# Kernel tuning notes

Hardware: AMD Instinct MI355X
Metric: run time of the kernel (lower is better)

Reference implementation:

```python
import jax, jax.numpy as jnp
import numpy as np

B, C, H, W = 8, 3, 1024, 1024
N, D, PS, NB, NH = 512, 256, 16, 8, 4


def _bin_matrix():
    # static radial-binning averaging matrix for a PS x (PS//2+1) rfft2 spectrum
    h, w = PS, PS // 2 + 1
    fy = np.fft.fftfreq(h)
    fx = np.linspace(0.0, 0.5, w)
    r = np.sqrt(fx[None, :] ** 2 + fy[:, None] ** 2)
    max_r = r.max() + 1e-6
    edges = np.linspace(0.0, max_r, NB + 1)
    idx = np.clip(np.searchsorted(edges, r.ravel(), side='right') - 1, 0, NB - 1)
    M = np.zeros((NB, h * w), np.float32)
    M[idx, np.arange(h * w)] = 1.0
    cnt = M.sum(1, keepdims=True)
    return M / np.maximum(cnt, 1.0)

_BIN_M = jnp.asarray(_bin_matrix())


def _ln(x, g, b, eps=1e-5):
    m = x.mean(-1, keepdims=True)
    v = x.var(-1, keepdims=True)
    return g * (x - m) / jnp.sqrt(v + eps) + b


def _gelu(x):
    return jax.nn.gelu(x, approximate=False)


def setup_inputs() -> dict:
    key = jax.random.key(0)
    ks = jax.random.split(key, 16)
    xav = lambda k, o, i: (jax.random.normal(k, (o, i)) / np.sqrt(i)).astype(jnp.float32)
    z = lambda n: jnp.zeros((n,), jnp.float32)
    o1 = lambda n: jnp.ones((n,), jnp.float32)
    FD = 2 * NB
    return {
        'image': jax.random.normal(ks[0], (B, C, H, W), jnp.float32),
        'point_coords': jax.random.uniform(ks[1], (B, N, 2), jnp.float32, 0.0, float(W)),
        'point_labels': jax.random.randint(ks[2], (B, N), 0, 2),
        'pe_w': xav(ks[3], D, D), 'pe_b': z(D),
        'type_emb': (0.02 * jax.random.normal(ks[4], (2, D))).astype(jnp.float32),
        'fbi': (1.0 + 0.1 * jax.random.normal(ks[5], (NB,))).astype(jnp.float32),
        'fe1_w': xav(ks[6], D // 2, FD), 'fe1_b': z(D // 2),
        'feln1_g': o1(D // 2), 'feln1_b': z(D // 2),
        'fe2_w': xav(ks[7], D, D // 2), 'fe2_b': z(D),
        'feln2_g': o1(D), 'feln2_b': z(D),
        'in_w': xav(ks[8], 3 * D, D), 'in_b': z(3 * D),
        'ao_w': xav(ks[9], D, D), 'ao_b': z(D),
        'n1_g': o1(D), 'n1_b': z(D),
        'f1_w': xav(ks[10], 2 * D, D), 'f1_b': z(2 * D),
        'f2_w': xav(ks[11], D, 2 * D), 'f2_b': z(D),
        'n2_g': o1(D), 'n2_b': z(D),
        'op_w': xav(ks[12], D, D), 'op_b': z(D),
    }


def reference(image, point_coords, point_labels, pe_w, pe_b, type_emb, fbi,
              fe1_w, fe1_b, feln1_g, feln1_b, fe2_w, fe2_b, feln2_g, feln2_b,
              in_w, in_b, ao_w, ao_b, n1_g, n1_b, f1_w, f1_b, f2_w, f2_b,
              n2_g, n2_b, op_w, op_b):
    Bv, Cv, Hv, Wv = image.shape
    Nv = point_coords.shape[1]
    # --- sinusoidal positional encoding (SAM style) + linear proj ---
    nc = point_coords / jnp.array([Wv, Hv], jnp.float32)
    dim_t = 10000.0 ** (2.0 * jnp.arange(D // 4, dtype=jnp.float32) / (D // 4))
    ax = (nc[..., 0:1] * (2.0 * np.pi)) / dim_t          # [B,N,D/4]
    ay = (nc[..., 1:2] * (2.0 * np.pi)) / dim_t
    pe = jnp.concatenate([jnp.sin(ax), jnp.cos(ax), jnp.sin(ay), jnp.cos(ay)], -1)
    spatial = pe @ pe_w.T + pe_b + type_emb[point_labels]  # [B,N,D]
    # --- batched per-point patch gather + rfft2 + radial binning ---
    gray = image.mean(1)                                   # [B,H,W]
    pc = jax.lax.stop_gradient(point_coords)               # .long() detaches in torch
    half = PS // 2
    px = jnp.clip(pc[..., 0].astype(jnp.int32), half, Wv - half - 1)
    py = jnp.clip(pc[..., 1].astype(jnp.int32), half, Hv - half - 1)
    off = jnp.arange(PS) - half
    rows = py[..., None] + off                             # [B,N,PS]
    cols = px[..., None] + off
    bidx = jnp.arange(Bv)[:, None, None, None]
    patches = gray[bidx, rows[..., :, None], cols[..., None, :]]  # [B,N,PS,PS]
    fft = jnp.fft.rfft2(patches, norm='ortho')             # [B,N,PS,PS//2+1]
    mag_bins = jnp.abs(fft).reshape(Bv, Nv, -1) @ _BIN_M.T    # [B,N,NB]
    ph_bins = jnp.angle(fft).reshape(Bv, Nv, -1) @ _BIN_M.T
    feat = jnp.concatenate([mag_bins * jax.nn.softmax(fbi), ph_bins], -1)  # [B,N,2*NB]
    # --- freq encoder MLP ---
    h1 = _gelu(_ln(feat @ fe1_w.T + fe1_b, feln1_g, feln1_b))
    freq = _ln(h1 @ fe2_w.T + fe2_b, feln2_g, feln2_b)     # [B,N,D]
    # --- cross-attention fusion (spatial = Q, freq = K/V) ---
    hd = D // NH
    q = (spatial @ in_w[:D].T + in_b[:D]).reshape(Bv, Nv, NH, hd)
    k = (freq @ in_w[D:2 * D].T + in_b[D:2 * D]).reshape(Bv, Nv, NH, hd)
    v = (freq @ in_w[2 * D:].T + in_b[2 * D:]).reshape(Bv, Nv, NH, hd)
    att = jax.nn.softmax(jnp.einsum('bqhd,bkhd->bhqk', q, k) / np.sqrt(hd), -1)
    o = jnp.einsum('bhqk,bkhd->bqhd', att, v).reshape(Bv, Nv, D)
    x = _ln(spatial + (o @ ao_w.T + ao_b), n1_g, n1_b)
    ffn = _gelu(x @ f1_w.T + f1_b) @ f2_w.T + f2_b
    x = _ln(x + ffn, n2_g, n2_b)
    return x @ op_w.T + op_b
```

## Files before the change

### kernel.cpp

```cpp
#include <hip/hip_runtime.h>
#include <math.h>


typedef __attribute__((ext_vector_type(8))) short short8;
typedef __attribute__((ext_vector_type(4))) float floatx4;
typedef unsigned short u16;
typedef unsigned long long u64;

__device__ __forceinline__ float gelu_f(float x) {
  return 0.5f * x * (1.0f + erff(x * 0.70710678118654752f));
}

__device__ __forceinline__ u16 bf16_rn(float x) {
  union { float f; unsigned u; } v; v.f = x;
  unsigned r = v.u + 0x7fffu + ((v.u >> 16) & 1u);
  return (u16)(r >> 16);
}

__device__ __forceinline__ void split_bf16(float x, u16& h, u16& l) {
  h = bf16_rn(x);
  union { unsigned u; float f; } hv; hv.u = ((unsigned)h) << 16;
  l = bf16_rn(x - hv.f);
}

#define W_PE   0
#define W_FE1  65536
#define W_FE2  67584
#define W_IN   100352
#define W_AO   296960
#define W_F1   362496
#define W_F2   493568
#define W_OP   624640


template <int NA, int K>
__device__ __forceinline__ void mm16_swz(
    const u16* Ah, const u16* Al, const int S,
    const u16* __restrict__ Bh, const u16* __restrict__ Bl,
    floatx4* acc)
{
  const int t = threadIdx.x;
  const int w = t >> 6, lane = t & 63;
  const int lm = lane & 15, kg = lane >> 4;
  #pragma unroll
  for (int it = 0; it < K / 32; ++it) {
    const short8 a_h = *(const short8*)&Ah[lm * S + it * 32 + kg * 8];
    const short8 a_l = *(const short8*)&Al[lm * S + it * 32 + kg * 8];
    #pragma unroll
    for (int nj = 0; nj < NA; nj++) {
      const size_t wo = (size_t)(((w * NA + nj) * (K / 32) + it) * 512 + lane * 8);
      const short8 b_h = *(const short8*)&Bh[wo];
      const short8 b_l = *(const short8*)&Bl[wo];
      acc[nj] = __builtin_amdgcn_mfma_f32_16x16x32_bf16(a_h, b_h, acc[nj], 0, 0, 0);
      acc[nj] = __builtin_amdgcn_mfma_f32_16x16x32_bf16(a_h, b_l, acc[nj], 0, 0, 0);
      acc[nj] = __builtin_amdgcn_mfma_f32_16x16x32_bf16(a_l, b_h, acc[nj], 0, 0, 0);
    }
  }
}

template <int NA, int K>
__device__ __forceinline__ void mm16_ks(
    const u16* Ah, const u16* Al, const int S,
    const u16* __restrict__ Bh, const u16* __restrict__ Bl,
    floatx4* acc)
{
  const int t = threadIdx.x;
  const int w = t >> 6, lane = t & 63;
  const int ww = w & 3, set = w >> 2;
  const int lm = lane & 15, kg = lane >> 4;
  #pragma unroll
  for (int itl = 0; itl < K / 128; ++itl) {
    const int it = set * (K / 128) + itl;
    const short8 a_h = *(const short8*)&Ah[lm * S + it * 32 + kg * 8];
    const short8 a_l = *(const short8*)&Al[lm * S + it * 32 + kg * 8];
    #pragma unroll
    for (int nj = 0; nj < NA; nj++) {
      const size_t wo = (size_t)(((ww * NA + nj) * (K / 32) + it) * 512 + lane * 8);
      const short8 b_h = *(const short8*)&Bh[wo];
      const short8 b_l = *(const short8*)&Bl[wo];
      acc[nj] = __builtin_amdgcn_mfma_f32_16x16x32_bf16(a_h, b_h, acc[nj], 0, 0, 0);
      acc[nj] = __builtin_amdgcn_mfma_f32_16x16x32_bf16(a_h, b_l, acc[nj], 0, 0, 0);
      acc[nj] = __builtin_amdgcn_mfma_f32_16x16x32_bf16(a_l, b_h, acc[nj], 0, 0, 0);
    }
  }
}

template <int NA>
__device__ __forceinline__ void reduce_sets(floatx4* acc, float* PART)
{
  const int t = threadIdx.x;
  const int w = t >> 6, lane = t & 63;
  const int ww = w & 3, set = w >> 2;
  const int lm = lane & 15, kg = lane >> 4;
  __syncthreads();
  if (set != 0) {
    #pragma unroll
    for (int nj = 0; nj < NA; nj++) {
      const int col = ww * (NA * 16) + nj * 16 + lm;
      #pragma unroll
      for (int r = 0; r < 4; r++)
        PART[((set - 1) * 16 + kg * 4 + r) * 260 + col] = acc[nj][r];
    }
  }
  __syncthreads();
  if (set == 0) {
    #pragma unroll
    for (int nj = 0; nj < NA; nj++) {
      const int col = ww * (NA * 16) + nj * 16 + lm;
      #pragma unroll
      for (int r = 0; r < 4; r++) {
        const int rr = kg * 4 + r;
        acc[nj][r] += PART[rr * 260 + col] + PART[(16 + rr) * 260 + col]
                    + PART[(32 + rr) * 260 + col];
      }
    }
  }
}

__device__ __forceinline__ void stage16(
    const u16* __restrict__ Gh, const u16* __restrict__ Gl,
    u16* Lh, u16* Ll)
{
  const int t = threadIdx.x;
  #pragma unroll
  for (int i = 0; i < 2; i++) {
    const int s = t + i * 256;
    const int row = s >> 5, c = (s & 31) * 8;
    *(short8*)&Lh[row * 264 + c] = *(const short8*)&Gh[(size_t)row * 256 + c];
    *(short8*)&Ll[row * 264 + c] = *(const short8*)&Gl[(size_t)row * 256 + c];
  }
  __syncthreads();
}

template <int N_, int NA>
__device__ __forceinline__ void ln_rows(const float (&v)[NA][4], float* red1, float* red2,
                                        float (&mean)[4], float (&rstd)[4])
{
  const int t = threadIdx.x;
  const int w = t >> 6;
  const int lane = t & 63;
  const int kg = lane >> 4;
  float s1[4] = {0.f,0.f,0.f,0.f}, s2[4] = {0.f,0.f,0.f,0.f};
  #pragma unroll
  for (int nj = 0; nj < NA; nj++)
    #pragma unroll
    for (int r = 0; r < 4; r++) { s1[r] += v[nj][r]; s2[r] += v[nj][r] * v[nj][r]; }
  #pragma unroll
  for (int r = 0; r < 4; r++) {
    #pragma unroll
    for (int off = 1; off < 16; off <<= 1) {
      s1[r] += __shfl_xor(s1[r], off);
      s2[r] += __shfl_xor(s2[r], off);
    }
  }
  __syncthreads();
  if ((lane & 15) == 0) {
    #pragma unroll
    for (int r = 0; r < 4; r++) {
      red1[w * 16 + kg * 4 + r] = s1[r];
      red2[w * 16 + kg * 4 + r] = s2[r];
    }
  }
  __syncthreads();
  #pragma unroll
  for (int r = 0; r < 4; r++) {
    const int rw = kg * 4 + r;
    const float a = red1[rw] + red1[16 + rw] + red1[32 + rw] + red1[48 + rw];
    const float b = red2[rw] + red2[16 + rw] + red2[32 + rw] + red2[48 + rw];
    mean[r] = a * (1.0f / N_);
    rstd[r] = rsqrtf(b * (1.0f / N_) - mean[r] * mean[r] + 1e-5f);
  }
}

template <int N_, int NA>
__device__ __forceinline__ void ln_rows16(const float (&v)[NA][4], float* red1, float* red2,
                                          float (&mean)[4], float (&rstd)[4])
{
  const int t = threadIdx.x;
  const int w = t >> 6;
  const int lane = t & 63;
  const int ww = w & 3, set = w >> 2;
  const int kg = lane >> 4;
  float s1[4] = {0.f,0.f,0.f,0.f}, s2[4] = {0.f,0.f,0.f,0.f};
  #pragma unroll
  for (int nj = 0; nj < NA; nj++)
    #pragma unroll
    for (int r = 0; r < 4; r++) { s1[r] += v[nj][r]; s2[r] += v[nj][r] * v[nj][r]; }
  #pragma unroll
  for (int r = 0; r < 4; r++) {
    #pragma unroll
    for (int off = 1; off < 16; off <<= 1) {
      s1[r] += __shfl_xor(s1[r], off);
      s2[r] += __shfl_xor(s2[r], off);
    }
  }
  __syncthreads();
  if (set == 0 && (lane & 15) == 0) {
    #pragma unroll
    for (int r = 0; r < 4; r++) {
      red1[ww * 16 + kg * 4 + r] = s1[r];
      red2[ww * 16 + kg * 4 + r] = s2[r];
    }
  }
  __syncthreads();
  if (set == 0) {
    #pragma unroll
    for (int r = 0; r < 4; r++) {
      const int rw = kg * 4 + r;
      const float a = red1[rw] + red1[16 + rw] + red1[32 + rw] + red1[48 + rw];
      const float b = red2[rw] + red2[16 + rw] + red2[32 + rw] + red2[48 + rw];
      mean[r] = a * (1.0f / N_);
      rstd[r] = rsqrtf(b * (1.0f / N_) - mean[r] * mean[r] + 1e-5f);
    }
  }
}

__device__ __forceinline__ void store_swz(
    u16* __restrict__ Wh, u16* __restrict__ Wl, const int segbase,
    const int rel, const int kshift, const float4 v)
{
  const int K = 1 << kshift;
  const int n = rel >> kshift;
  const int k = rel & (K - 1);
  const int off8 = ((n >> 4) * (K >> 5) + (k >> 5)) * 512
                 + (((k >> 3) & 3) * 16 + (n & 15)) * 8 + (k & 7);
  u16 h0,h1,h2,h3,l0,l1,l2,l3;
  split_bf16(v.x,h0,l0); split_bf16(v.y,h1,l1);
  split_bf16(v.z,h2,l2); split_bf16(v.w,h3,l3);
  *(u64*)&Wh[segbase + off8] = (u64)h0 | ((u64)h1<<16) | ((u64)h2<<32) | ((u64)h3<<48);
  *(u64*)&Wl[segbase + off8] = (u64)l0 | ((u64)l1<<16) | ((u64)l2<<32) | ((u64)l3<<48);
}

__global__ __launch_bounds__(64) void k0_prep(
    const float* __restrict__ image, const float* __restrict__ coords,
    const float* __restrict__ fbi,
    const float* __restrict__ pe_w, const float* __restrict__ fe1_w,
    const float* __restrict__ fe2_w, const float* __restrict__ in_w,
    const float* __restrict__ ao_w, const float* __restrict__ f1_w,
    const float* __restrict__ f2_w, const float* __restrict__ op_w,
    u16* __restrict__ Wh, u16* __restrict__ Wl,
    u16* __restrict__ PEh, u16* __restrict__ PEl,
    u16* __restrict__ FEATh, u16* __restrict__ FEATl)
{
  const int blk = blockIdx.x;
  const int lane = threadIdx.x;

  if (blk < 2696) {
    const int idx = (blk * 64 + lane) * 4;
    if (idx < W_FE1) {
      store_swz(Wh, Wl, W_PE, idx - W_PE, 8, *(const float4*)&pe_w[idx - W_PE]);
    } else if (idx < W_FE2) {
      const int rel = idx - W_FE1;
      const float4 v = *(const float4*)&fe1_w[rel];
      u16 h0,h1,h2,h3,l0,l1,l2,l3;
      split_bf16(v.x,h0,l0); split_bf16(v.y,h1,l1);
      split_bf16(v.z,h2,l2); split_bf16(v.w,h3,l3);
      *(u64*)&Wh[idx] = (u64)h0 | ((u64)h1<<16) | ((u64)h2<<32) | ((u64)h3<<48);
      *(u64*)&Wl[idx] = (u64)l0 | ((u64)l1<<16) | ((u64)l2<<32) | ((u64)l3<<48);
    } else if (idx < W_IN) {
      store_swz(Wh, Wl, W_FE2, idx - W_FE2, 7, *(const float4*)&fe2_w[idx - W_FE2]);
    } else if (idx < W_AO) {
      store_swz(Wh, Wl, W_IN, idx - W_IN, 8, *(const float4*)&in_w[idx - W_IN]);
    } else if (idx < W_F1) {
      store_swz(Wh, Wl, W_AO, idx - W_AO, 8, *(const float4*)&ao_w[idx - W_AO]);
    } else if (idx < W_F2) {
      store_swz(Wh, Wl, W_F1, idx - W_F1, 8, *(const float4*)&f1_w[idx - W_F1]);
    } else if (idx < W_OP) {
      store_swz(Wh, Wl, W_F2, idx - W_F2, 9, *(const float4*)&f2_w[idx - W_F2]);
    } else {
      store_swz(Wh, Wl, W_OP, idx - W_OP, 8, *(const float4*)&op_w[idx - W_OP]);
    }
    return;
  }

  const int id = blk - 2696;
  const int b  = id >> 9;
  const float pcx = coords[id * 2 + 0];
  const float pcy = coords[id * 2 + 1];

  {
    const float TWO_PI = 6.283185307179586f;
    const float dimt = expf((float)lane * 0.28782313662425572f);
    const float ax = (pcx * (1.0f / 1024.0f)) * TWO_PI / dimt;
    const float ay = (pcy * (1.0f / 1024.0f)) * TWO_PI / dimt;
    u16 h, l;
    split_bf16(sinf(ax), h, l); PEh[id*256+lane]     = h; PEl[id*256+lane]     = l;
    split_bf16(cosf(ax), h, l); PEh[id*256+lane+64]  = h; PEl[id*256+lane+64]  = l;
    split_bf16(sinf(ay), h, l); PEh[id*256+lane+128] = h; PEl[id*256+lane+128] = l;
    split_bf16(cosf(ay), h, l); PEh[id*256+lane+192] = h; PEl[id*256+lane+192] = l;
  }

  int px = (int)pcx; px = px < 8 ? 8 : (px > 1015 ? 1015 : px);
  int py = (int)pcy; py = py < 8 ? 8 : (py > 1015 ? 1015 : py);

  __shared__ float patch[256];
  __shared__ float ct[16], st[16];
  __shared__ float Gre[144], Gim[144];
  __shared__ float msum[8], psum[8];
  __shared__ int cnt8[8];
  {
    const float* img = image + (size_t)b * 3145728;
    #pragma unroll
    for (int i = 0; i < 4; i++) {
      const int p = i * 64 + lane;
      const int r = p >> 4, c = p & 15;
      const int off = (py - 8 + r) * 1024 + (px - 8 + c);
      const float s = img[off] + img[off + 1048576] + img[off + 2097152];
      patch[r * 16 + c] = s * (1.0f / 3.0f);
    }
  }
  if (lane < 16) {
    float c, s;
    if ((lane & 3) == 0) {
      const float cv[4] = {1.0f, 0.0f, -1.0f, 0.0f};
      const float sv[4] = {0.0f, -1.0f, 0.0f, 1.0f};
      c = cv[lane >> 2]; s = sv[lane >> 2];
    } else {
      const float a = -3.14159265358979f * (float)lane * 0.125f;
      c = cosf(a); s = sinf(a);
    }
    ct[lane] = c; st[lane] = s;
  }
  if (lane < 8) { msum[lane] = 0.0f; psum[lane] = 0.0f; cnt8[lane] = 0; }
  __syncthreads();

  for (int tt = lane; tt < 144; tt += 64) {
    const int y = tt / 9, kx = tt - y * 9;
    float re = 0.0f, im = 0.0f;
    #pragma unroll
    for (int x = 0; x < 16; x++) {
      const int w = (x * kx) & 15;
      const float pv = patch[y * 16 + x];
      re = fmaf(pv, ct[w], re);
      im = fmaf(pv, st[w], im);
    }
    Gre[tt] = re; Gim[tt] = im;
  }
  __syncthreads();

  for (int tt = lane; tt < 144; tt += 64) {
    const int ky = tt / 9, kx = tt - ky * 9;
    float re = 0.0f, im = 0.0f;
    #pragma unroll
    for (int y = 0; y < 16; y++) {
      const int w = (y * ky) & 15;
      const float gr = Gre[y * 9 + kx], gi = Gim[y * 9 + kx];
      re = fmaf(gr, ct[w], re);
      re = fmaf(-gi, st[w], re);
      im = fmaf(gr, st[w], im);
      im = fmaf(gi, ct[w], im);
    }
    if (((ky & 7) == 0) && ((kx & 7) == 0)) im = 0.0f;
    const float mag = sqrtf(re * re + im * im) * 0.0625f;
    const float ph  = atan2f(im, re);

    const float fy = (ky < 8) ? (float)ky * 0.0625f : (float)(ky - 16) * 0.0625f;
    const float fx = (float)kx * 0.0625f;
    const float r = sqrtf(fx * fx + fy * fy);
    const float max_r = 0.7071077811865476f;
    const float stepf = max_r * 0.125f;
    int idx = 0;
    #pragma unroll
    for (int kq = 1; kq <= 8; kq++) {
      const float e = (kq == 8) ? max_r : stepf * (float)kq;
      if (r >= e) idx = kq;
    }
    if (idx > 7) idx = 7;
    atomicAdd(&msum[idx], mag);
    atomicAdd(&psum[idx], ph);
    atomicAdd(&cnt8[idx], 1);
  }
  __syncthreads();

  if (lane < 8) {
    float fm = fbi[0];
    #pragma unroll
    for (int j = 1; j < 8; j++) fm = fmaxf(fm, fbi[j]);
    float se = 0.0f;
    #pragma unroll
    for (int j = 0; j < 8; j++) se += expf(fbi[j] - fm);
    const float smx = expf(fbi[lane] - fm) / se;
    const float c = (float)(cnt8[lane] > 0 ? cnt8[lane] : 1);
    u16 h, l;
    split_bf16((msum[lane] / c) * smx, h, l);
    FEATh[id*16+lane] = h; FEATl[id*16+lane] = l;
    split_bf16(psum[lane] / c, h, l);
    FEATh[id*16+8+lane] = h; FEATl[id*16+8+lane] = l;
  }
}

__global__ __launch_bounds__(256) void k1_front(
    const u16* __restrict__ Wh, const u16* __restrict__ Wl,
    const u16* __restrict__ PEh, const u16* __restrict__ PEl,
    const u16* __restrict__ FEATh, const u16* __restrict__ FEATl,
    const float* __restrict__ pe_b, const int* __restrict__ labels,
    const float* __restrict__ temb,
    const float* __restrict__ fe1_b, const float* __restrict__ feln1_g, const float* __restrict__ feln1_b,
    const float* __restrict__ fe2_b, const float* __restrict__ feln2_g, const float* __restrict__ feln2_b,
    float* __restrict__ SPATIAL32, u16* __restrict__ SPh, u16* __restrict__ SPl,
    u16* __restrict__ FQh, u16* __restrict__ FQl)
{
  __shared__ __align__(16) u16 smem[8448];
  __shared__ float redbuf[128];
  const int blk = blockIdx.x;
  const int t = threadIdx.x;
  const int w = t >> 6, lane = t & 63;
  const int lm = lane & 15, kg = lane >> 4;

  if (blk < 256) {
    const int m0 = blk * 16;
    u16* Lh = smem;
    u16* Ll = smem + 4224;
    stage16(PEh + (size_t)m0 * 256, PEl + (size_t)m0 * 256, Lh, Ll);
    floatx4 acc[4];
    #pragma unroll
    for (int j = 0; j < 4; j++) acc[j] = (floatx4){0.f,0.f,0.f,0.f};
    mm16_swz<4, 256>(Lh, Ll, 264, Wh + W_PE, Wl + W_PE, acc);
    #pragma unroll
    for (int nj = 0; nj < 4; nj++) {
      const int col = w * 64 + nj * 16 + lm;
      #pragma unroll
      for (int r = 0; r < 4; r++) {
        const int row = m0 + kg * 4 + r;
        const float v = acc[nj][r] + pe_b[col] + temb[labels[row] * 256 + col];
        SPATIAL32[(size_t)row * 256 + col] = v;
        u16 h, l; split_bf16(v, h, l);
        SPh[(size_t)row * 256 + col] = h;
        SPl[(size_t)row * 256 + col] = l;
      }
    }
    return;
  }

  const int m0 = (blk - 256) * 16;
  u16* h1h = smem;
  u16* h1l = smem + 2176;

  floatx4 acc1[2];
  acc1[0] = (floatx4){0.f,0.f,0.f,0.f};
  acc1[1] = (floatx4){0.f,0.f,0.f,0.f};
  {
    const short8 zz = {0,0,0,0,0,0,0,0};
    const short8 a_h = (kg < 2) ? *(const short8*)&FEATh[(size_t)(m0 + lm) * 16 + kg * 8] : zz;
    const short8 a_l = (kg < 2) ? *(const short8*)&FEATl[(size_t)(m0 + lm) * 16 + kg * 8] : zz;
    #pragma unroll
    for (int nj = 0; nj < 2; nj++) {
      const int col = w * 32 + nj * 16 + lm;
      const short8 b_h = (kg < 2) ? *(const short8*)&Wh[W_FE1 + (size_t)col * 16 + kg * 8] : zz;
      const short8 b_l = (kg < 2) ? *(const short8*)&Wl[W_FE1 + (size_t)col * 16 + kg * 8] : zz;
      acc1[nj] = __builtin_amdgcn_mfma_f32_16x16x32_bf16(a_h, b_h, acc1[nj], 0, 0, 0);
      acc1[nj] = __builtin_amdgcn_mfma_f32_16x16x32_bf16(a_h, b_l, acc1[nj], 0, 0, 0);
      acc1[nj] = __builtin_amdgcn_mfma_f32_16x16x32_bf16(a_l, b_h, acc1[nj], 0, 0, 0);
    }
  }

  float v1[2][4];
  #pragma unroll
  for (int nj = 0; nj < 2; nj++) {
    const int col = w * 32 + nj * 16 + lm;
    #pragma unroll
    for (int r = 0; r < 4; r++) v1[nj][r] = acc1[nj][r] + fe1_b[col];
  }
  float mean[4], rstd[4];
  ln_rows<128, 2>(v1, redbuf, redbuf + 64, mean, rstd);
  #pragma unroll
  for (int nj = 0; nj < 2; nj++) {
    const int col = w * 32 + nj * 16 + lm;
    #pragma unroll
    for (int r = 0; r < 4; r++) {
      float y = feln1_g[col] * (v1[nj][r] - mean[r]) * rstd[r] + feln1_b[col];
      y = gelu_f(y);
      u16 h, l; split_bf16(y, h, l);
      h1h[(kg * 4 + r) * 136 + col] = h;
      h1l[(kg * 4 + r) * 136 + col] = l;
    }
  }
  __syncthreads();

  floatx4 acc2[4];
  #pragma unroll
  for (int j = 0; j < 4; j++) acc2[j] = (floatx4){0.f,0.f,0.f,0.f};
  mm16_swz<4, 128>(h1h, h1l, 136, Wh + W_FE2, Wl + W_FE2, acc2);

  float v2[4][4];
  #pragma unroll
  for (int nj = 0; nj < 4; nj++) {
    const int col = w * 64 + nj * 16 + lm;
    #pragma unroll
    for (int r = 0; r < 4; r++) v2[nj][r] = acc2[nj][r] + fe2_b[col];
  }
  ln_rows<256, 4>(v2, redbuf, redbuf + 64, mean, rstd);
  #pragma unroll
  for (int nj = 0; nj < 4; nj++) {
    const int col = w * 64 + nj * 16 + lm;
    #pragma unroll
    for (int r = 0; r < 4; r++) {
      const int rw = m0 + kg * 4 + r;
      float y = feln2_g[col] * (v2[nj][r] - mean[r]) * rstd[r] + feln2_b[col];
      u16 h, l; split_bf16(y, h, l);
      FQh[(size_t)rw * 256 + col] = h;
      FQl[(size_t)rw * 256 + col] = l;
    }
  }
}

__global__ __launch_bounds__(256) void k2_qkv(
    const u16* __restrict__ Wh, const u16* __restrict__ Wl,
    const u16* __restrict__ SPh, const u16* __restrict__ SPl,
    const u16* __restrict__ FQh, const u16* __restrict__ FQl,
    const float* __restrict__ in_b,
    u16* __restrict__ Qh, u16* __restrict__ Ql,
    u16* __restrict__ Kh, u16* __restrict__ Kl,
    u16* __restrict__ Vth, u16* __restrict__ Vtl)
{
  __shared__ __align__(16) u16 smem[8448];
  const int bx = blockIdx.x;
  const int seg = bx >> 8;
  const int m0 = (bx & 255) * 16;
  const int t = threadIdx.x;
  const int w = t >> 6, lane = t & 63;
  const int lm = lane & 15, kg = lane >> 4;

  const u16 *Ah, *Al; const u16 *Wsh, *Wsl; const float* bias;
  if (seg == 0)      { Ah = SPh; Al = SPl; Wsh = Wh + W_IN;          Wsl = Wl + W_IN;          bias = in_b; }
  else if (seg == 1) { Ah = FQh; Al = FQl; Wsh = Wh + W_IN + 65536;  Wsl = Wl + W_IN + 65536;  bias = in_b + 256; }
  else               { Ah = FQh; Al = FQl; Wsh = Wh + W_IN + 131072; Wsl = Wl + W_IN + 131072; bias = in_b + 512; }

  u16* Lh = smem;
  u16* Ll = smem + 4224;
  stage16(Ah + (size_t)m0 * 256, Al + (size_t)m0 * 256, Lh, Ll);

  floatx4 acc[4];
  #pragma unroll
  for (int j = 0; j < 4; j++) acc[j] = (floatx4){0.f,0.f,0.f,0.f};
  mm16_swz<4, 256>(Lh, Ll, 264, Wsh, Wsl, acc);

  if (seg < 2) {
    u16* oh = (seg == 0) ? Qh : Kh;
    u16* ol = (seg == 0) ? Ql : Kl;
    #pragma unroll
    for (int nj = 0; nj < 4; nj++) {
      const int col = w * 64 + nj * 16 + lm;
      #pragma unroll
      for (int r = 0; r < 4; r++) {
        const int row = m0 + kg * 4 + r;
        u16 h, l; split_bf16(acc[nj][r] + bias[col], h, l);
        oh[(size_t)row * 256 + col] = h;
        ol[(size_t)row * 256 + col] = l;
      }
    }
  } else {
    #pragma unroll
    for (int nj = 0; nj < 4; nj++) {
      const int col = w * 64 + nj * 16 + lm;
      u64 hp = 0, lp = 0;
      #pragma unroll
      for (int r = 0; r < 4; r++) {
        u16 h, l; split_bf16(acc[nj][r] + bias[col], h, l);
        hp |= ((u64)h) << (16 * r);
        lp |= ((u64)l) << (16 * r);
      }
      *(u64*)&Vth[(size_t)col * 4096 + m0 + kg * 4] = hp;
      *(u64*)&Vtl[(size_t)col * 4096 + m0 + kg * 4] = lp;
    }
  }
}

__global__ __launch_bounds__(512) void k3_attn(
    const u16* __restrict__ Qh, const u16* __restrict__ Ql,
    const u16* __restrict__ Kh, const u16* __restrict__ Kl,
    const u16* __restrict__ Vth, const u16* __restrict__ Vtl,
    u16* __restrict__ Oh, u16* __restrict__ Ol)
{
  __shared__ __align__(16) u16 smem[64512];
  __shared__ float O1[64 * 68];
  __shared__ float Mbuf[64], Lbuf[64];

  const int t = threadIdx.x;
  const int w = t >> 6, lane = t & 63;
  const int ww = w & 3, set = w >> 2;
  const int lm = lane & 15, kg = lane >> 4;
  const int ts = t & 255;

  u16* sQh = smem;
  u16* sQl = smem + 4608;
  u16* sKh = smem + 9216 + set * 27648;
  u16* sKl = sKh + 4608;
  u16* sVh = sKh + 9216;
  u16* sVl = sKh + 13824;
  u16* sPh = sKh + 18432;
  u16* sPl = sKh + 23040;

  const int qt = blockIdx.x & 7;
  const int bh = blockIdx.x >> 3;
  const int b = bh >> 2, h = bh & 3;
  const int qrow0 = b * 512 + qt * 64;

  {
    const int r = t >> 3, d = (t & 7) * 8;
    *(short8*)&sQh[r * 72 + d] = *(const short8*)&Qh[(size_t)(qrow0 + r) * 256 + h * 64 + d];
    *(short8*)&sQl[r * 72 + d] = *(const short8*)&Ql[(size_t)(qrow0 + r) * 256 + h * 64 + d];
  }

  float m_i[4], l_i[4];
  floatx4 o_acc[4];
  #pragma unroll
  for (int r = 0; r < 4; r++) { m_i[r] = -INFINITY; l_i[r] = 0.0f; }
  #pragma unroll
  for (int dj = 0; dj < 4; dj++) o_acc[dj] = (floatx4){0.f, 0.f, 0.f, 0.f};

  __syncthreads();
  short8 q_h[2], q_l[2];
  #pragma unroll
  for (int ks = 0; ks < 2; ks++) {
    const int off = (ww * 16 + lm) * 72 + ks * 32 + kg * 8;
    q_h[ks] = *(const short8*)&sQh[off];
    q_l[ks] = *(const short8*)&sQl[off];
  }

  for (int ktl = 0; ktl < 4; ktl++) {
    const int kt = set * 4 + ktl;
    __syncthreads();
    {
      const int krow0 = b * 512 + kt * 64;
      #pragma unroll
      for (int i = 0; i < 2; i++) {
        const int s = ts + i * 256;
        const int r = s >> 3, d = (s & 7) * 8;
        *(short8*)&sKh[r * 72 + d] = *(const short8*)&Kh[(size_t)(krow0 + r) * 256 + h * 64 + d];
        *(short8*)&sKl[r * 72 + d] = *(const short8*)&Kl[(size_t)(krow0 + r) * 256 + h * 64 + d];
        *(short8*)&sVh[r * 72 + d] = *(const short8*)&Vth[(size_t)(h * 64 + r) * 4096 + krow0 + d];
        *(short8*)&sVl[r * 72 + d] = *(const short8*)&Vtl[(size_t)(h * 64 + r) * 4096 + krow0 + d];
      }
    }
    __syncthreads();

    floatx4 sacc[4];
    #pragma unroll
    for (int nj = 0; nj < 4; nj++) sacc[nj] = (floatx4){0.f, 0.f, 0.f, 0.f};
    #pragma unroll
    for (int ks = 0; ks < 2; ks++) {
      #pragma unroll
      for (int nj = 0; nj < 4; nj++) {
        const int off = (nj * 16 + lm) * 72 + ks * 32 + kg * 8;
        const short8 kb_h = *(const short8*)&sKh[off];
        const short8 kb_l = *(const short8*)&sKl[off];
        sacc[nj] = __builtin_amdgcn_mfma_f32_16x16x32_bf16(q_h[ks], kb_h, sacc[nj], 0, 0, 0);
        sacc[nj] = __builtin_amdgcn_mfma_f32_16x16x32_bf16(q_h[ks], kb_l, sacc[nj], 0, 0, 0);
        sacc[nj] = __builtin_amdgcn_mfma_f32_16x16x32_bf16(q_l[ks], kb_h, sacc[nj], 0, 0, 0);
      }
    }

    float pp[4][4];
    #pragma unroll
    for (int r = 0; r < 4; r++) {
      float mx = -INFINITY;
      #pragma unroll
      for (int nj = 0; nj < 4; nj++) {
        sacc[nj][r] *= 0.125f;
        mx = fmaxf(mx, sacc[nj][r]);
      }
      #pragma unroll
      for (int off = 1; off < 16; off <<= 1) mx = fmaxf(mx, __shfl_xor(mx, off));
      const float mnew = fmaxf(m_i[r], mx);
      const float alpha = expf(m_i[r] - mnew);
      m_i[r] = mnew;
      float rs = 0.0f;
      #pragma unroll
      for (int nj = 0; nj < 4; nj++) { pp[nj][r] = expf(sacc[nj][r] - mnew); rs += pp[nj][r]; }
      #pragma unroll
      for (int off = 1; off < 16; off <<= 1) rs += __shfl_xor(rs, off);
      l_i[r] = l_i[r] * alpha + rs;
      #pragma unroll
      for (int dj = 0; dj < 4; dj++) o_acc[dj][r] *= alpha;
    }

    #pragma unroll
    for (int nj = 0; nj < 4; nj++)
      #pragma unroll
      for (int r = 0; r < 4; r++) {
        u16 ph, pl; split_bf16(pp[nj][r], ph, pl);
        sPh[(ww * 16 + kg * 4 + r) * 72 + nj * 16 + lm] = ph;
        sPl[(ww * 16 + kg * 4 + r) * 72 + nj * 16 + lm] = pl;
      }

    #pragma unroll
    for (int ks = 0; ks < 2; ks++) {
      const short8 p_h = *(const short8*)&sPh[(ww * 16 + lm) * 72 + ks * 32 + kg * 8];
      const short8 p_l = *(const short8*)&sPl[(ww * 16 + lm) * 72 + ks * 32 + kg * 8];
      #pragma unroll
      for (int dj = 0; dj < 4; dj++) {
        const int off = (dj * 16 + lm) * 72 + ks * 32 + kg * 8;
        const short8 v_h = *(const short8*)&sVh[off];
        const short8 v_l = *(const short8*)&sVl[off];
        o_acc[dj] = __builtin_amdgcn_mfma_f32_16x16x32_bf16(p_h, v_h, o_acc[dj], 0, 0, 0);
        o_acc[dj] = __builtin_amdgcn_mfma_f32_16x16x32_bf16(p_l, v_h, o_acc[dj], 0, 0, 0);
        o_acc[dj] = __builtin_amdgcn_mfma_f32_16x16x32_bf16(p_h, v_l, o_acc[dj], 0, 0, 0);
      }
    }
  }

  if (set == 1) {
    #pragma unroll
    for (int r = 0; r < 4; r++) {
      const int row = ww * 16 + kg * 4 + r;
      if (lm == 0) { Mbuf[row] = m_i[r]; Lbuf[row] = l_i[r]; }
      #pragma unroll
      for (int dj = 0; dj < 4; dj++)
        O1[row * 68 + dj * 16 + lm] = o_acc[dj][r];
    }
  }
  __syncthreads();
  if (set == 0) {
    #pragma unroll
    for (int r = 0; r < 4; r++) {
      const int row = ww * 16 + kg * 4 + r;
      const float m1 = Mbuf[row], l1v = Lbuf[row];
      const float mnew = fmaxf(m_i[r], m1);
      const float a0 = expf(m_i[r] - mnew);
      const float a1 = expf(m1 - mnew);
      const float inv_l = 1.0f / (l_i[r] * a0 + l1v * a1);
      const size_t rowoff = (size_t)(qrow0 + row) * 256 + h * 64;
      #pragma unroll
      for (int dj = 0; dj < 4; dj++) {
        const float val = (o_acc[dj][r] * a0 + O1[row * 68 + dj * 16 + lm] * a1) * inv_l;
        u16 hh, ll; split_bf16(val, hh, ll);
        Oh[rowoff + dj * 16 + lm] = hh;
        Ol[rowoff + dj * 16 + lm] = ll;
      }
    }
  }
}

__global__ __launch_bounds__(1024) void k4_tail(
    const u16* __restrict__ Wh, const u16* __restrict__ Wl,
    const u16* __restrict__ Oh, const u16* __restrict__ Ol,
    const float* __restrict__ SPATIAL32,
    const float* __restrict__ ao_b, const float* __restrict__ n1_g, const float* __restrict__ n1_b,
    const float* __restrict__ f1_b, const float* __restrict__ f2_b,
    const float* __restrict__ n2_g, const float* __restrict__ n2_b,
    const float* __restrict__ op_b, float* __restrict__ OUT)
{
  __shared__ __align__(16) u16 smem[25088];
  __shared__ float redbuf[128];
  __shared__ float PART[3 * 16 * 260];
  u16* B1h = smem;
  u16* B1l = smem + 4224;
  u16* Fh  = smem + 8448;
  u16* Fl  = smem + 16768;

  const int t = threadIdx.x;
  const int w = t >> 6, lane = t & 63;
  const int ww = w & 3, set = w >> 2;
  const int lm = lane & 15, kg = lane >> 4;
  const int m0 = blockIdx.x * 16;

  {
    const u16* Gh = Oh + (size_t)m0 * 256;
    const u16* Gl = Ol + (size_t)m0 * 256;
    if (t < 512) {
      const int row = t >> 5, c = (t & 31) * 8;
      *(short8*)&B1h[row * 264 + c] = *(const short8*)&Gh[(size_t)row * 256 + c];
      *(short8*)&B1l[row * 264 + c] = *(const short8*)&Gl[(size_t)row * 256 + c];
    }
    __syncthreads();
  }

  floatx4 acc[4];
  #pragma unroll
  for (int j = 0; j < 4; j++) acc[j] = (floatx4){0.f,0.f,0.f,0.f};
  mm16_ks<4, 256>(B1h, B1l, 264, Wh + W_AO, Wl + W_AO, acc);
  reduce_sets<4>(acc, PART);

  float x1reg[4][4];
  {
    float v[4][4];
    if (set == 0) {
      #pragma unroll
      for (int nj = 0; nj < 4; nj++) {
        const int col = ww * 64 + nj * 16 + lm;
        #pragma unroll
        for (int r = 0; r < 4; r++)
          v[nj][r] = acc[nj][r] + ao_b[col] + SPATIAL32[(size_t)(m0 + kg * 4 + r) * 256 + col];
      }
    } else {
      #pragma unroll
      for (int nj = 0; nj < 4; nj++)
        #pragma unroll
        for (int r = 0; r < 4; r++) v[nj][r] = 0.0f;
    }
    float mean[4], rstd[4];
    ln_rows16<256, 4>(v, redbuf, redbuf + 64, mean, rstd);
    if (set == 0) {
      #pragma unroll
      for (int nj = 0; nj < 4; nj++) {
        const int col = ww * 64 + nj * 16 + lm;
        #pragma unroll
        for (int r = 0; r < 4; r++) {
          const float y = n1_g[col] * (v[nj][r] - mean[r]) * rstd[r] + n1_b[col];
          x1reg[nj][r] = y;
          u16 h, l; split_bf16(y, h, l);
          B1h[(kg * 4 + r) * 264 + col] = h;
          B1l[(kg * 4 + r) * 264 + col] = l;
        }
      }
    }
  }
  __syncthreads();

  #pragma unroll
  for (int ct = 0; ct < 2; ct++) {
    floatx4 a4[4];
    #pragma unroll
    for (int j = 0; j < 4; j++) a4[j] = (floatx4){0.f,0.f,0.f,0.f};
    mm16_ks<4, 256>(B1h, B1l, 264,
                    Wh + W_F1 + (size_t)ct * 65536, Wl + W_F1 + (size_t)ct * 65536, a4);
    reduce_sets<4>(a4, PART);
    if (set == 0) {
      #pragma unroll
      for (int nj = 0; nj < 4; nj++) {
        const int col = ct * 256 + ww * 64 + nj * 16 + lm;
        #pragma unroll
        for (int r = 0; r < 4; r++) {
          const float y = gelu_f(a4[nj][r] + f1_b[col]);
          u16 h, l; split_bf16(y, h, l);
          Fh[(kg * 4 + r) * 520 + col] = h;
          Fl[(kg * 4 + r) * 520 + col] = l;
        }
      }
    }
  }
  __syncthreads();

  #pragma unroll
  for (int j = 0; j < 4; j++) acc[j] = (floatx4){0.f,0.f,0.f,0.f};
  mm16_ks<4, 512>(Fh, Fl, 520, Wh + W_F2, Wl + W_F2, acc);
  reduce_sets<4>(acc, PART);
  {
    float v[4][4];
    if (set == 0) {
      #pragma unroll
      for (int nj = 0; nj < 4; nj++) {
        const int col = ww * 64 + nj * 16 + lm;
        #pragma unroll
        for (int r = 0; r < 4; r++)
          v[nj][r] = acc[nj][r] + f2_b[col] + x1reg[nj][r];
      }
    } else {
      #pragma unroll
      for (int nj = 0; nj < 4; nj++)
        #pragma unroll
        for (int r = 0; r < 4; r++) v[nj][r] = 0.0f;
    }
    float mean[4], rstd[4];
    ln_rows16<256, 4>(v, redbuf, redbuf + 64, mean, rstd);
    if (set == 0) {
      #pragma unroll
      for (int nj = 0; nj < 4; nj++) {
        const int col = ww * 64 + nj * 16 + lm;
        #pragma unroll
        for (int r = 0; r < 4; r++) {
          const float y = n2_g[col] * (v[nj][r] - mean[r]) * rstd[r] + n2_b[col];
          u16 h, l; split_bf16(y, h, l);
          B1h[(kg * 4 + r) * 264 + col] = h;
          B1l[(kg * 4 + r) * 264 + col] = l;
        }
      }
    }
  }
  __syncthreads();

  #pragma unroll
  for (int j = 0; j < 4; j++) acc[j] = (floatx4){0.f,0.f,0.f,0.f};
  mm16_ks<4, 256>(B1h, B1l, 264, Wh + W_OP, Wl + W_OP, acc);
  reduce_sets<4>(acc, PART);
  if (set == 0) {
    #pragma unroll
    for (int nj = 0; nj < 4; nj++) {
      const int col = ww * 64 + nj * 16 + lm;
      #pragma unroll
      for (int r = 0; r < 4; r++)
        OUT[(size_t)(m0 + kg * 4 + r) * 256 + col] = acc[nj][r] + op_b[col];
    }
  }
}

extern "C" void kernel_launch(void* const* d_in, const int* in_sizes, int n_in,
                              void* d_out, int out_size, void* d_ws, size_t ws_size,
                              hipStream_t stream) {
  const float* image   = (const float*)d_in[0];
  const float* coords  = (const float*)d_in[1];
  const int*   labels  = (const int*)d_in[2];
  const float* pe_w    = (const float*)d_in[3];
  const float* pe_b    = (const float*)d_in[4];
  const float* temb    = (const float*)d_in[5];
  const float* fbi     = (const float*)d_in[6];
  const float* fe1_w   = (const float*)d_in[7];
  const float* fe1_b   = (const float*)d_in[8];
  const float* feln1_g = (const float*)d_in[9];
  const float* feln1_b = (const float*)d_in[10];
  const float* fe2_w   = (const float*)d_in[11];
  const float* fe2_b   = (const float*)d_in[12];
  const float* feln2_g = (const float*)d_in[13];
  const float* feln2_b = (const float*)d_in[14];
  const float* in_w    = (const float*)d_in[15];
  const float* in_b    = (const float*)d_in[16];
  const float* ao_w    = (const float*)d_in[17];
  const float* ao_b    = (const float*)d_in[18];
  const float* n1_g    = (const float*)d_in[19];
  const float* n1_b    = (const float*)d_in[20];
  const float* f1_w    = (const float*)d_in[21];
  const float* f1_b    = (const float*)d_in[22];
  const float* f2_w    = (const float*)d_in[23];
  const float* f2_b    = (const float*)d_in[24];
  const float* n2_g    = (const float*)d_in[25];
  const float* n2_b    = (const float*)d_in[26];
  const float* op_w    = (const float*)d_in[27];
  const float* op_b    = (const float*)d_in[28];

  float* ws = (float*)d_ws;
  float* SPATIAL32 = ws;
  u16* S = (u16*)(ws + 2 * (1u << 20));
  u16* Wh = S;
  u16* Wl = S + 690176;
  u16* PEh   = S + 1380352;  u16* PEl   = PEh + 1048576;
  u16* FEATh = S + 3477504;  u16* FEATl = FEATh + 65536;
  u16* FQh   = S + 4657152;  u16* FQl   = FQh + 1048576;
  u16* SPh   = S + 6754304;  u16* SPl   = SPh + 1048576;
  u16* Qh    = S + 8851456;  u16* Ql    = Qh + 1048576;
  u16* Kh    = S + 10948608; u16* Kl    = Kh + 1048576;
  u16* Vth   = S + 13045760; u16* Vtl   = Vth + 1048576;
  u16* Oh    = S + 15142912; u16* Ol    = Oh + 1048576;

  float* OUT = (float*)d_out;

  k0_prep<<<6792, 64, 0, stream>>>(
      image, coords, fbi, pe_w, fe1_w, fe2_w, in_w, ao_w, f1_w, f2_w, op_w,
      Wh, Wl, PEh, PEl, FEATh, FEATl);
  k1_front<<<512, 256, 0, stream>>>(
      Wh, Wl, PEh, PEl, FEATh, FEATl, pe_b, labels, temb,
      fe1_b, feln1_g, feln1_b, fe2_b, feln2_g, feln2_b,
      SPATIAL32, SPh, SPl, FQh, FQl);
  k2_qkv<<<768, 256, 0, stream>>>(
      Wh, Wl, SPh, SPl, FQh, FQl, in_b, Qh, Ql, Kh, Kl, Vth, Vtl);
  k3_attn<<<256, 512, 0, stream>>>(Qh, Ql, Kh, Kl, Vth, Vtl, Oh, Ol);
  k4_tail<<<256, 1024, 0, stream>>>(
      Wh, Wl, Oh, Ol, SPATIAL32, ao_b, n1_g, n1_b, f1_b, f2_b, n2_g, n2_b, op_b, OUT);
}
```

Measured before the change: 287.1 us.

## Split attention key halves across blocks and merge partials in tail kernel

The attention kernel now runs 512 blocks of 256 threads, each handling one half of the keys. Each block writes unnormalised fp32 partial outputs plus per-row max and sum to workspace, and the tail kernel merges the two halves with flash-style rescaling while staging its input. The QKV projection kernel also moves to 512 threads, splitting K across two wave sets with a shared-memory reduction. This is meant to raise occupancy and parallelism, at the cost of extra fp32 global traffic for the partial outputs and an added reduction step.

```diff
diff --git a/kernel.cpp b/kernel.cpp
--- a/kernel.cpp
+++ b/kernel.cpp
@@ -58,7 +58,7 @@
   }
 }
 
-template <int NA, int K>
+template <int NA, int K, int NSETS>
 __device__ __forceinline__ void mm16_ks(
     const u16* Ah, const u16* Al, const int S,
     const u16* __restrict__ Bh, const u16* __restrict__ Bl,
@@ -68,9 +68,10 @@
   const int w = t >> 6, lane = t & 63;
   const int ww = w & 3, set = w >> 2;
   const int lm = lane & 15, kg = lane >> 4;
-  #pragma unroll
-  for (int itl = 0; itl < K / 128; ++itl) {
-    const int it = set * (K / 128) + itl;
+  constexpr int ITERS = K / (32 * NSETS);
+  #pragma unroll
+  for (int itl = 0; itl < ITERS; ++itl) {
+    const int it = set * ITERS + itl;
     const short8 a_h = *(const short8*)&Ah[lm * S + it * 32 + kg * 8];
     const short8 a_l = *(const short8*)&Al[lm * S + it * 32 + kg * 8];
     #pragma unroll
@@ -113,6 +114,35 @@
         acc[nj][r] += PART[rr * 260 + col] + PART[(16 + rr) * 260 + col]
                     + PART[(32 + rr) * 260 + col];
       }
+    }
+  }
+}
+
+template <int NA>
+__device__ __forceinline__ void reduce_sets2(floatx4* acc, float* PART)
+{
+  const int t = threadIdx.x;
+  const int w = t >> 6, lane = t & 63;
+  const int ww = w & 3, set = w >> 2;
+  const int lm = lane & 15, kg = lane >> 4;
+  __syncthreads();
+  if (set == 1) {
+    #pragma unroll
+    for (int nj = 0; nj < NA; nj++) {
+      const int col = ww * (NA * 16) + nj * 16 + lm;
+      #pragma unroll
+      for (int r = 0; r < 4; r++)
+        PART[(kg * 4 + r) * 260 + col] = acc[nj][r];
+    }
+  }
+  __syncthreads();
+  if (set == 0) {
+    #pragma unroll
+    for (int nj = 0; nj < NA; nj++) {
+      const int col = ww * (NA * 16) + nj * 16 + lm;
+      #pragma unroll
+      for (int r = 0; r < 4; r++)
+        acc[nj][r] += PART[(kg * 4 + r) * 260 + col];
     }
   }
 }
@@ -504,7 +534,7 @@
   }
 }
 
-__global__ __launch_bounds__(256) void k2_qkv(
+__global__ __launch_bounds__(512) void k2_qkv(
     const u16* __restrict__ Wh, const u16* __restrict__ Wl,
     const u16* __restrict__ SPh, const u16* __restrict__ SPl,
     const u16* __restrict__ FQh, const u16* __restrict__ FQl,
@@ -514,11 +544,13 @@
     u16* __restrict__ Vth, u16* __restrict__ Vtl)
 {
   __shared__ __align__(16) u16 smem[8448];
+  __shared__ float PART[16 * 260];
   const int bx = blockIdx.x;
   const int seg = bx >> 8;
   const int m0 = (bx & 255) * 16;
   const int t = threadIdx.x;
   const int w = t >> 6, lane = t & 63;
+  const int ww = w & 3, set = w >> 2;
   const int lm = lane & 15, kg = lane >> 4;
 
   const u16 *Ah, *Al; const u16 *Wsh, *Wsl; const float* bias;
@@ -528,19 +560,29 @@
 
   u16* Lh = smem;
   u16* Ll = smem + 4224;
-  stage16(Ah + (size_t)m0 * 256, Al + (size_t)m0 * 256, Lh, Ll);
+  {
+    const u16* Gh = Ah + (size_t)m0 * 256;
+    const u16* Gl = Al + (size_t)m0 * 256;
+    const int row = t >> 5, c = (t & 31) * 8;
+    *(short8*)&Lh[row * 264 + c] = *(const short8*)&Gh[(size_t)row * 256 + c];
+    *(short8*)&Ll[row * 264 + c] = *(const short8*)&Gl[(size_t)row * 256 + c];
+    __syncthreads();
+  }
 
   floatx4 acc[4];
   #pragma unroll
   for (int j = 0; j < 4; j++) acc[j] = (floatx4){0.f,0.f,0.f,0.f};
-  mm16_swz<4, 256>(Lh, Ll, 264, Wsh, Wsl, acc);
+  mm16_ks<4, 256, 2>(Lh, Ll, 264, Wsh, Wsl, acc);
+  reduce_sets2<4>(acc, PART);
+
+  if (set != 0) return;
 
   if (seg < 2) {
     u16* oh = (seg == 0) ? Qh : Kh;
     u16* ol = (seg == 0) ? Ql : Kl;
     #pragma unroll
     for (int nj = 0; nj < 4; nj++) {
-      const int col = w * 64 + nj * 16 + lm;
+      const int col = ww * 64 + nj * 16 + lm;
       #pragma unroll
       for (int r = 0; r < 4; r++) {
         const int row = m0 + kg * 4 + r;
@@ -552,7 +594,7 @@
   } else {
     #pragma unroll
     for (int nj = 0; nj < 4; nj++) {
-      const int col = w * 64 + nj * 16 + lm;
+      const int col = ww * 64 + nj * 16 + lm;
       u64 hp = 0, lp = 0;
       #pragma unroll
       for (int r = 0; r < 4; r++) {
@@ -566,38 +608,36 @@
   }
 }
 
-__global__ __launch_bounds__(512) void k3_attn(
+__global__ __launch_bounds__(256) void k3_attn(
     const u16* __restrict__ Qh, const u16* __restrict__ Ql,
     const u16* __restrict__ Kh, const u16* __restrict__ Kl,
     const u16* __restrict__ Vth, const u16* __restrict__ Vtl,
-    u16* __restrict__ Oh, u16* __restrict__ Ol)
-{
-  __shared__ __align__(16) u16 smem[64512];
-  __shared__ float O1[64 * 68];
-  __shared__ float Mbuf[64], Lbuf[64];
-
+    float* __restrict__ OP, float* __restrict__ ML)
+{
+  __shared__ __align__(16) u16 smem[36864];
+  u16* sQh = smem;
+  u16* sQl = smem + 4608;
+  u16* sKh = smem + 9216;
+  u16* sKl = smem + 13824;
+  u16* sVh = smem + 18432;
+  u16* sVl = smem + 23040;
+  u16* sPh = smem + 27648;
+  u16* sPl = smem + 32256;
+
+  const int bx = blockIdx.x;
+  const int half = bx & 1;
+  const int qt = (bx >> 1) & 7;
+  const int bh = bx >> 4;
+  const int b = bh >> 2, h = bh & 3;
   const int t = threadIdx.x;
   const int w = t >> 6, lane = t & 63;
-  const int ww = w & 3, set = w >> 2;
   const int lm = lane & 15, kg = lane >> 4;
-  const int ts = t & 255;
-
-  u16* sQh = smem;
-  u16* sQl = smem + 4608;
-  u16* sKh = smem + 9216 + set * 27648;
-  u16* sKl = sKh + 4608;
-  u16* sVh = sKh + 9216;
-  u16* sVl = sKh + 13824;
-  u16* sPh = sKh + 18432;
-  u16* sPl = sKh + 23040;
-
-  const int qt = blockIdx.x & 7;
-  const int bh = blockIdx.x >> 3;
-  const int b = bh >> 2, h = bh & 3;
   const int qrow0 = b * 512 + qt * 64;
 
-  {
-    const int r = t >> 3, d = (t & 7) * 8;
+  #pragma unroll
+  for (int i = 0; i < 2; i++) {
+    const int s = t + i * 256;
+    const int r = s >> 3, d = (s & 7) * 8;
     *(short8*)&sQh[r * 72 + d] = *(const short8*)&Qh[(size_t)(qrow0 + r) * 256 + h * 64 + d];
     *(short8*)&sQl[r * 72 + d] = *(const short8*)&Ql[(size_t)(qrow0 + r) * 256 + h * 64 + d];
   }
@@ -613,19 +653,19 @@
   short8 q_h[2], q_l[2];
   #pragma unroll
   for (int ks = 0; ks < 2; ks++) {
-    const int off = (ww * 16 + lm) * 72 + ks * 32 + kg * 8;
+    const int off = (w * 16 + lm) * 72 + ks * 32 + kg * 8;
     q_h[ks] = *(const short8*)&sQh[off];
     q_l[ks] = *(const short8*)&sQl[off];
   }
 
   for (int ktl = 0; ktl < 4; ktl++) {
-    const int kt = set * 4 + ktl;
+    const int kt = half * 4 + ktl;
     __syncthreads();
     {
       const int krow0 = b * 512 + kt * 64;
       #pragma unroll
       for (int i = 0; i < 2; i++) {
-        const int s = ts + i * 256;
+        const int s = t + i * 256;
         const int r = s >> 3, d = (s & 7) * 8;
         *(short8*)&sKh[r * 72 + d] = *(const short8*)&Kh[(size_t)(krow0 + r) * 256 + h * 64 + d];
         *(short8*)&sKl[r * 72 + d] = *(const short8*)&Kl[(size_t)(krow0 + r) * 256 + h * 64 + d];
@@ -680,14 +720,14 @@
       #pragma unroll
       for (int r = 0; r < 4; r++) {
         u16 ph, pl; split_bf16(pp[nj][r], ph, pl);
-        sPh[(ww * 16 + kg * 4 + r) * 72 + nj * 16 + lm] = ph;
-        sPl[(ww * 16 + kg * 4 + r) * 72 + nj * 16 + lm] = pl;
+        sPh[(w * 16 + kg * 4 + r) * 72 + nj * 16 + lm] = ph;
+        sPl[(w * 16 + kg * 4 + r) * 72 + nj * 16 + lm] = pl;
       }
 
     #pragma unroll
     for (int ks = 0; ks < 2; ks++) {
-      const short8 p_h = *(const short8*)&sPh[(ww * 16 + lm) * 72 + ks * 32 + kg * 8];
-      const short8 p_l = *(const short8*)&sPl[(ww * 16 + lm) * 72 + ks * 32 + kg * 8];
+      const short8 p_h = *(const short8*)&sPh[(w * 16 + lm) * 72 + ks * 32 + kg * 8];
+      const short8 p_l = *(const short8*)&sPl[(w * 16 + lm) * 72 + ks * 32 + kg * 8];
       #pragma unroll
       for (int dj = 0; dj < 4; dj++) {
         const int off = (dj * 16 + lm) * 72 + ks * 32 + kg * 8;
@@ -700,41 +740,23 @@
     }
   }
 
-  if (set == 1) {
-    #pragma unroll
-    for (int r = 0; r < 4; r++) {
-      const int row = ww * 16 + kg * 4 + r;
-      if (lm == 0) { Mbuf[row] = m_i[r]; Lbuf[row] = l_i[r]; }
-      #pragma unroll
-      for (int dj = 0; dj < 4; dj++)
-        O1[row * 68 + dj * 16 + lm] = o_acc[dj][r];
-    }
-  }
-  __syncthreads();
-  if (set == 0) {
-    #pragma unroll
-    for (int r = 0; r < 4; r++) {
-      const int row = ww * 16 + kg * 4 + r;
-      const float m1 = Mbuf[row], l1v = Lbuf[row];
-      const float mnew = fmaxf(m_i[r], m1);
-      const float a0 = expf(m_i[r] - mnew);
-      const float a1 = expf(m1 - mnew);
-      const float inv_l = 1.0f / (l_i[r] * a0 + l1v * a1);
-      const size_t rowoff = (size_t)(qrow0 + row) * 256 + h * 64;
-      #pragma unroll
-      for (int dj = 0; dj < 4; dj++) {
-        const float val = (o_acc[dj][r] * a0 + O1[row * 68 + dj * 16 + lm] * a1) * inv_l;
-        u16 hh, ll; split_bf16(val, hh, ll);
-        Oh[rowoff + dj * 16 + lm] = hh;
-        Ol[rowoff + dj * 16 + lm] = ll;
-      }
-    }
+  #pragma unroll
+  for (int r = 0; r < 4; r++) {
+    const int row = w * 16 + kg * 4 + r;
+    const int grow = qrow0 + row;
+    if (lm == 0) {
+      ML[half * 32768 + grow * 8 + h * 2]     = m_i[r];
+      ML[half * 32768 + grow * 8 + h * 2 + 1] = l_i[r];
+    }
+    #pragma unroll
+    for (int dj = 0; dj < 4; dj++)
+      OP[(size_t)half * 1048576 + (size_t)grow * 256 + h * 64 + dj * 16 + lm] = o_acc[dj][r];
   }
 }
 
 __global__ __launch_bounds__(1024) void k4_tail(
     const u16* __restrict__ Wh, const u16* __restrict__ Wl,
-    const u16* __restrict__ Oh, const u16* __restrict__ Ol,
+    const float* __restrict__ OP, const float* __restrict__ ML,
     const float* __restrict__ SPATIAL32,
     const float* __restrict__ ao_b, const float* __restrict__ n1_g, const float* __restrict__ n1_b,
     const float* __restrict__ f1_b, const float* __restrict__ f2_b,
@@ -756,12 +778,40 @@
   const int m0 = blockIdx.x * 16;
 
   {
-    const u16* Gh = Oh + (size_t)m0 * 256;
-    const u16* Gl = Ol + (size_t)m0 * 256;
     if (t < 512) {
-      const int row = t >> 5, c = (t & 31) * 8;
-      *(short8*)&B1h[row * 264 + c] = *(const short8*)&Gh[(size_t)row * 256 + c];
-      *(short8*)&B1l[row * 264 + c] = *(const short8*)&Gl[(size_t)row * 256 + c];
+      const int row = t >> 5, cg = t & 31;
+      const int c = cg * 8;
+      const int hh_ = cg >> 3;
+      const int grow = m0 + row;
+      const float m0v = ML[grow * 8 + hh_ * 2],         l0v = ML[grow * 8 + hh_ * 2 + 1];
+      const float m1v = ML[32768 + grow * 8 + hh_ * 2], l1v = ML[32768 + grow * 8 + hh_ * 2 + 1];
+      const float mn = fmaxf(m0v, m1v);
+      const float a0 = expf(m0v - mn), a1 = expf(m1v - mn);
+      const float inv = 1.0f / (l0v * a0 + l1v * a1);
+      const float4 v0a = *(const float4*)&OP[(size_t)grow * 256 + c];
+      const float4 v0b = *(const float4*)&OP[(size_t)grow * 256 + c + 4];
+      const float4 v1a = *(const float4*)&OP[1048576 + (size_t)grow * 256 + c];
+      const float4 v1b = *(const float4*)&OP[1048576 + (size_t)grow * 256 + c + 4];
+      const float mv[8] = {
+        (v0a.x * a0 + v1a.x * a1) * inv, (v0a.y * a0 + v1a.y * a1) * inv,
+        (v0a.z * a0 + v1a.z * a1) * inv, (v0a.w * a0 + v1a.w * a1) * inv,
+        (v0b.x * a0 + v1b.x * a1) * inv, (v0b.y * a0 + v1b.y * a1) * inv,
+        (v0b.z * a0 + v1b.z * a1) * inv, (v0b.w * a0 + v1b.w * a1) * inv };
+      u64 ph0 = 0, pl0 = 0, ph1 = 0, pl1 = 0;
+      #pragma unroll
+      for (int i = 0; i < 4; i++) {
+        u16 hx, lx; split_bf16(mv[i], hx, lx);
+        ph0 |= ((u64)hx) << (16 * i); pl0 |= ((u64)lx) << (16 * i);
+      }
+      #pragma unroll
+      for (int i = 0; i < 4; i++) {
+        u16 hx, lx; split_bf16(mv[4 + i], hx, lx);
+        ph1 |= ((u64)hx) << (16 * i); pl1 |= ((u64)lx) << (16 * i);
+      }
+      *(u64*)&B1h[row * 264 + c]     = ph0;
+      *(u64*)&B1h[row * 264 + c + 4] = ph1;
+      *(u64*)&B1l[row * 264 + c]     = pl0;
+      *(u64*)&B1l[row * 264 + c + 4] = pl1;
     }
     __syncthreads();
   }
@@ -769,7 +819,7 @@
   floatx4 acc[4];
   #pragma unroll
   for (int j = 0; j < 4; j++) acc[j] = (floatx4){0.f,0.f,0.f,0.f};
-  mm16_ks<4, 256>(B1h, B1l, 264, Wh + W_AO, Wl + W_AO, acc);
+  mm16_ks<4, 256, 4>(B1h, B1l, 264, Wh + W_AO, Wl + W_AO, acc);
   reduce_sets<4>(acc, PART);
 
   float x1reg[4][4];
@@ -813,8 +863,8 @@
     floatx4 a4[4];
     #pragma unroll
     for (int j = 0; j < 4; j++) a4[j] = (floatx4){0.f,0.f,0.f,0.f};
-    mm16_ks<4, 256>(B1h, B1l, 264,
-                    Wh + W_F1 + (size_t)ct * 65536, Wl + W_F1 + (size_t)ct * 65536, a4);
+    mm16_ks<4, 256, 4>(B1h, B1l, 264,
+                       Wh + W_F1 + (size_t)ct * 65536, Wl + W_F1 + (size_t)ct * 65536, a4);
     reduce_sets<4>(a4, PART);
     if (set == 0) {
       #pragma unroll
@@ -834,7 +884,7 @@
 
   #pragma unroll
   for (int j = 0; j < 4; j++) acc[j] = (floatx4){0.f,0.f,0.f,0.f};
-  mm16_ks<4, 512>(Fh, Fl, 520, Wh + W_F2, Wl + W_F2, acc);
+  mm16_ks<4, 512, 4>(Fh, Fl, 520, Wh + W_F2, Wl + W_F2, acc);
   reduce_sets<4>(acc, PART);
   {
     float v[4][4];
@@ -872,7 +922,7 @@
 
   #pragma unroll
   for (int j = 0; j < 4; j++) acc[j] = (floatx4){0.f,0.f,0.f,0.f};
-  mm16_ks<4, 256>(B1h, B1l, 264, Wh + W_OP, Wl + W_OP, acc);
+  mm16_ks<4, 256, 4>(B1h, B1l, 264, Wh + W_OP, Wl + W_OP, acc);
   reduce_sets<4>(acc, PART);
   if (set == 0) {
     #pragma unroll
@@ -930,7 +980,8 @@
   u16* Qh    = S + 8851456;  u16* Ql    = Qh + 1048576;
   u16* Kh    = S + 10948608; u16* Kl    = Kh + 1048576;
   u16* Vth   = S + 13045760; u16* Vtl   = Vth + 1048576;
-  u16* Oh    = S + 15142912; u16* Ol    = Oh + 1048576;
+  float* OP  = (float*)(S + 15142912);
+  float* ML  = (float*)(S + 19337216);
 
   float* OUT = (float*)d_out;
 
@@ -941,9 +992,9 @@
       Wh, Wl, PEh, PEl, FEATh, FEATl, pe_b, labels, temb,
       fe1_b, feln1_g, feln1_b, fe2_b, feln2_g, feln2_b,
       SPATIAL32, SPh, SPl, FQh, FQl);
-  k2_qkv<<<768, 256, 0, stream>>>(
+  k2_qkv<<<768, 512, 0, stream>>>(
       Wh, Wl, SPh, SPl, FQh, FQl, in_b, Qh, Ql, Kh, Kl, Vth, Vtl);
-  k3_attn<<<256, 512, 0, stream>>>(Qh, Ql, Kh, Kl, Vth, Vtl, Oh, Ol);
+  k3_attn<<<512, 256, 0, stream>>>(Qh, Ql, Kh, Kl, Vth, Vtl, OP, ML);
   k4_tail<<<256, 1024, 0, stream>>>(
-      Wh, Wl, Oh, Ol, SPATIAL32, ao_b, n1_g, n1_b, f1_b, f2_b, n2_g, n2_b, op_b, OUT);
-}
+      Wh, Wl, OP, ML, SPATIAL32, ao_b, n1_g, n1_b, f1_b, f2_b, n2_g, n2_b, op_b, OUT);
+}
```

New measurement: 306.3 us. 1.07x slower.
